# Kernel tuning notes

Measured on AMD Instinct MI355X. Metric: run time of the kernel, lower is better.

The kernel has to match this reference:

```python
import jax, jax.numpy as jnp
import numpy as np

# Dims fixed by ExpertC.__init__ defaults
INPUT_DIM, HIDDEN, OUT_DIM, NLAYERS = 1024, 256, 256, 2
D_STATE, EXPAND, HEADDIM = 32, 2, 32
D_INNER = EXPAND * HIDDEN                      # 512
NHEADS = D_INNER // HEADDIM                    # 16
CONV_DIM = D_INNER + 2 * D_STATE               # 576 (x, B, C; ngroups=1)
D_IN_PROJ = 2 * D_INNER + 2 * D_STATE + NHEADS # 1104 (z, xBC, dt)
KCONV = 4
B, L = 16, 2048
EPS = 1e-5


def setup_inputs() -> dict:
    key = jax.random.key(0)
    ks = iter(jax.random.split(key, 40))
    rn = lambda shape, s: jax.random.normal(next(ks), shape, jnp.float32) * s
    inp = {}
    inp["x"] = rn((B, L, INPUT_DIM), 1.0)
    inp["ip_w"] = rn((INPUT_DIM, HIDDEN), INPUT_DIM ** -0.5)
    inp["ip_b"] = jnp.zeros((HIDDEN,), jnp.float32)
    inp["m_inw"] = rn((NLAYERS, HIDDEN, D_IN_PROJ), HIDDEN ** -0.5)
    inp["m_inb"] = jnp.zeros((NLAYERS, D_IN_PROJ), jnp.float32)
    inp["m_convw"] = rn((NLAYERS, CONV_DIM, KCONV), 0.3)
    inp["m_convb"] = jnp.zeros((NLAYERS, CONV_DIM), jnp.float32)
    inp["m_dtb"] = rn((NLAYERS, NHEADS), 0.5)
    inp["m_Alog"] = jnp.log(1.0 + 15.0 * jax.random.uniform(next(ks), (NLAYERS, NHEADS), jnp.float32))
    inp["m_D"] = jnp.ones((NLAYERS, NHEADS), jnp.float32)
    inp["m_nw"] = jnp.ones((NLAYERS, D_INNER), jnp.float32)
    inp["m_outw"] = rn((NLAYERS, D_INNER, HIDDEN), D_INNER ** -0.5)
    inp["m_outb"] = jnp.zeros((NLAYERS, HIDDEN), jnp.float32)
    inp["rms_w"] = jnp.ones((NLAYERS, HIDDEN), jnp.float32)
    inp["ln1_w"] = jnp.ones((HIDDEN,), jnp.float32)
    inp["ln1_b"] = jnp.zeros((HIDDEN,), jnp.float32)
    inp["w1"] = rn((HIDDEN, 2 * HIDDEN), HIDDEN ** -0.5)
    inp["b1"] = jnp.zeros((2 * HIDDEN,), jnp.float32)
    inp["w2"] = rn((2 * HIDDEN, OUT_DIM), (2 * HIDDEN) ** -0.5)
    inp["b2"] = jnp.zeros((OUT_DIM,), jnp.float32)
    inp["ln2_w"] = jnp.ones((OUT_DIM,), jnp.float32)
    inp["ln2_b"] = jnp.zeros((OUT_DIM,), jnp.float32)
    return inp


def rmsnorm(x, w):
    return x * jax.lax.rsqrt(jnp.mean(x * x, axis=-1, keepdims=True) + EPS) * w


def layernorm(x, w, b):
    m = jnp.mean(x, axis=-1, keepdims=True)
    v = jnp.mean((x - m) ** 2, axis=-1, keepdims=True)
    return (x - m) * jax.lax.rsqrt(v + EPS) * w + b


def mamba_layer(x, inw, inb, convw, convb, dtb, Alog, D, nw, outw, outb):
    b, l, _ = x.shape
    zxbcdt = x @ inw + inb                                   # (b,l,1104)
    z, xBC, dt = jnp.split(zxbcdt, [D_INNER, D_INNER + CONV_DIM], axis=-1)
    dt = jax.nn.softplus(dt + dtb)                           # (b,l,h)
    # causal depthwise conv1d (kernel 4) + silu
    xp = jnp.pad(xBC, ((0, 0), (KCONV - 1, 0), (0, 0)))
    xBC = sum(xp[:, i:i + l, :] * convw[:, i] for i in range(KCONV)) + convb
    xBC = jax.nn.silu(xBC)
    xs, Bm, Cm = jnp.split(xBC, [D_INNER, D_INNER + D_STATE], axis=-1)
    xh = xs.reshape(b, l, NHEADS, HEADDIM)                   # (b,l,h,p)
    A = -jnp.exp(Alog)                                       # (h,)
    dA = jnp.exp(dt * A)                                     # (b,l,h)
    dtx = dt[..., None] * xh                                 # (b,l,h,p)

    def step(h, inp):
        dA_t, dtx_t, B_t, C_t = inp
        # h: (b,h,p,n)
        h = h * dA_t[:, :, None, None] + dtx_t[..., None] * B_t[:, None, None, :]
        y = jnp.einsum('bhpn,bn->bhp', h, C_t)
        return h, y

    h0 = jnp.zeros((b, NHEADS, HEADDIM, D_STATE), x.dtype)
    xs_t = (jnp.moveaxis(dA, 1, 0), jnp.moveaxis(dtx, 1, 0),
            jnp.moveaxis(Bm, 1, 0), jnp.moveaxis(Cm, 1, 0))
    _, ys = jax.lax.scan(step, h0, xs_t)                     # (l,b,h,p)
    y = jnp.moveaxis(ys, 0, 1) + D[None, None, :, None] * xh
    y = y.reshape(b, l, D_INNER)
    y = rmsnorm(y * jax.nn.silu(z), nw)                      # gated RMSNorm
    return y @ outw + outb


def _expert(x, ip_w, ip_b, m_inw, m_inb, m_convw, m_convb, m_dtb, m_Alog, m_D,
            m_nw, m_outw, m_outb, rms_w, ln1_w, ln1_b, w1, b1, w2, b2, ln2_w, ln2_b):
    if x.ndim == 2:
        x = x[:, None, :]
    x = x @ ip_w + ip_b
    for i in range(NLAYERS):
        res = x
        x = mamba_layer(x, m_inw[i], m_inb[i], m_convw[i], m_convb[i], m_dtb[i],
                        m_Alog[i], m_D[i], m_nw[i], m_outw[i], m_outb[i])
        x = rmsnorm(x + res, rms_w[i])
    x = layernorm(x, ln1_w, ln1_b)
    x = jax.nn.gelu(x @ w1 + b1, approximate=False)          # dropout is eval no-op
    x = x @ w2 + b2
    return layernorm(x, ln2_w, ln2_b)


def reference(x, ip_w, ip_b, m_inw, m_inb, m_convw, m_convb, m_dtb, m_Alog, m_D,
              m_nw, m_outw, m_outb, rms_w, ln1_w, ln1_b, w1, b1, w2, b2, ln2_w, ln2_b):
    return _expert(x, ip_w, ip_b, m_inw, m_inb, m_convw, m_convb, m_dtb, m_Alog, m_D,
                   m_nw, m_outw, m_outb, rms_w, ln1_w, ln1_b, w1, b1, w2, b2, ln2_w, ln2_b)
```

## Files before the change

### kernel.cpp

```cpp
#include <hip/hip_runtime.h>

typedef __bf16 bf16;
typedef __bf16 bf16x8 __attribute__((ext_vector_type(8)));
typedef float  f32x4  __attribute__((ext_vector_type(4)));

#define EPSF 1e-5f

__device__ __forceinline__ float bf2f(bf16 x) { return (float)x; }
__device__ __forceinline__ bf16  f2bf(float x) { return (bf16)x; }
__device__ __forceinline__ float siluf(float x) { return x / (1.f + expf(-x)); }

struct PrepackArgs {
    const float* W[7];
    bf16* TH[7];
    bf16* TL[7];
    int K[7];
    int N[7];
};

__global__ __launch_bounds__(256) void prepack_kernel(PrepackArgs a)
{
    int s = blockIdx.y;
    int idx = blockIdx.x * 256 + threadIdx.x;
    int K = a.K[s], N = a.N[s];
    if (idx >= K * N) return;
    int k = idx / N, n = idx - k * N;
    float v = a.W[s][idx];
    bf16 hi = f2bf(v);
    a.TH[s][(size_t)n * K + k] = hi;
    a.TL[s][(size_t)n * K + k] = f2bf(v - bf2f(hi));
}

__global__ __launch_bounds__(256) void gemm_hl(
    const bf16* __restrict__ AH, const bf16* __restrict__ AL,
    const float* __restrict__ Af, int lda,
    const bf16* __restrict__ WTh, const bf16* __restrict__ WTl,
    const float* __restrict__ bias,
    int N, int K,
    float* __restrict__ outF, int ldF,
    bf16* __restrict__ outB, int ldB,
    bf16* __restrict__ outH, bf16* __restrict__ outL, int ldH,
    int doGelu,
    const float* __restrict__ dtb, const float* __restrict__ Alog,
    float* __restrict__ dtf, float* __restrict__ dAf)
{
    __shared__ bf16 As [128][40];
    __shared__ bf16 Als[128][40];

    const int tid  = threadIdx.x;
    const int lane = tid & 63;
    const int wid  = tid >> 6;
    const int waveM = wid & 1, waveN = wid >> 1;
    const int m16 = lane & 15, quad = lane >> 4;
    const int row0 = blockIdx.x * 128;
    const int n0   = blockIdx.y * 64;

    f32x4 acc[4][2];
#pragma unroll
    for (int i = 0; i < 4; ++i)
#pragma unroll
        for (int j = 0; j < 2; ++j)
            acc[i][j] = (f32x4){0.f, 0.f, 0.f, 0.f};

    const int ar = tid >> 1, akc = (tid & 1) * 16;

    const int bn0 = min(n0 + waveN * 32 + m16,      N - 1);
    const int bn1 = min(n0 + waveN * 32 + 16 + m16, N - 1);
    const bf16* bH0p = WTh + (size_t)bn0 * K + quad * 8;
    const bf16* bH1p = WTh + (size_t)bn1 * K + quad * 8;
    const bf16* bL0p = WTl + (size_t)bn0 * K + quad * 8;
    const bf16* bL1p = WTl + (size_t)bn1 * K + quad * 8;

    bf16x8 bH[2], bL[2], bHn[2], bLn[2];
    bH[0] = *(const bf16x8*)(bH0p);
    bH[1] = *(const bf16x8*)(bH1p);
    bL[0] = *(const bf16x8*)(bL0p);
    bL[1] = *(const bf16x8*)(bL1p);

    for (int k0 = 0; k0 < K; k0 += 32) {
        if (AH) {
            const bf16* s0 = AH + (size_t)(row0 + ar) * lda + k0 + akc;
            const bf16* s1 = AL + (size_t)(row0 + ar) * lda + k0 + akc;
            *(uint4*)&As [ar][akc]     = *(const uint4*)s0;
            *(uint4*)&As [ar][akc + 8] = *(const uint4*)(s0 + 8);
            *(uint4*)&Als[ar][akc]     = *(const uint4*)s1;
            *(uint4*)&Als[ar][akc + 8] = *(const uint4*)(s1 + 8);
        } else {
            const float* asrc = Af + (size_t)(row0 + ar) * lda + k0 + akc;
            bf16* dh = &As [ar][akc];
            bf16* dl = &Als[ar][akc];
#pragma unroll
            for (int c = 0; c < 4; ++c) {
                float4 f = ((const float4*)asrc)[c];
#pragma unroll
                for (int e = 0; e < 4; ++e) {
                    float v = (&f.x)[e];
                    bf16 hi = f2bf(v);
                    dh[c * 4 + e] = hi;
                    dl[c * 4 + e] = f2bf(v - bf2f(hi));
                }
            }
        }
        __syncthreads();

        const bool more = (k0 + 32) < K;
        if (more) {
            int kn = k0 + 32;
            bHn[0] = *(const bf16x8*)(bH0p + kn);
            bHn[1] = *(const bf16x8*)(bH1p + kn);
            bLn[0] = *(const bf16x8*)(bL0p + kn);
            bLn[1] = *(const bf16x8*)(bL1p + kn);
        }

        bf16x8 aH[4], aL[4];
#pragma unroll
        for (int mi = 0; mi < 4; ++mi) {
            aH[mi] = *(const bf16x8*)&As [waveM * 64 + mi * 16 + m16][quad * 8];
            aL[mi] = *(const bf16x8*)&Als[waveM * 64 + mi * 16 + m16][quad * 8];
        }

#pragma unroll
        for (int mi = 0; mi < 4; ++mi)
#pragma unroll
            for (int ni = 0; ni < 2; ++ni) {
                acc[mi][ni] = __builtin_amdgcn_mfma_f32_16x16x32_bf16(
                    aH[mi], bH[ni], acc[mi][ni], 0, 0, 0);
                acc[mi][ni] = __builtin_amdgcn_mfma_f32_16x16x32_bf16(
                    aH[mi], bL[ni], acc[mi][ni], 0, 0, 0);
                acc[mi][ni] = __builtin_amdgcn_mfma_f32_16x16x32_bf16(
                    aL[mi], bH[ni], acc[mi][ni], 0, 0, 0);
            }
        __syncthreads();

        if (more) {
            bH[0] = bHn[0]; bH[1] = bHn[1];
            bL[0] = bLn[0]; bL[1] = bLn[1];
        }
    }

#pragma unroll
    for (int ni = 0; ni < 2; ++ni) {
        int col = n0 + waveN * 32 + ni * 16 + m16;
        if (col >= N) continue;
        float bv = bias ? bias[col] : 0.f;
#pragma unroll
        for (int mi = 0; mi < 4; ++mi) {
#pragma unroll
            for (int r = 0; r < 4; ++r) {
                int row = row0 + waveM * 64 + mi * 16 + quad * 4 + r;
                float v = acc[mi][ni][r] + bv;
                if (dtf && col >= 1088) {
                    int head = col - 1088;
                    float xx = v + dtb[head];
                    float sp = (xx > 20.f) ? xx : log1pf(expf(xx));
                    float A  = -expf(Alog[head]);
                    dtf[(size_t)row * 16 + head] = sp;
                    dAf[(size_t)row * 16 + head] = expf(sp * A);
                } else {
                    if (doGelu) v = 0.5f * v * (1.f + erff(v * 0.70710678118654752f));
                    if (outB) outB[(size_t)row * ldB + col] = f2bf(v);
                    if (outF) outF[(size_t)row * ldF + col] = v;
                    if (outH) {
                        bf16 hi = f2bf(v);
                        outH[(size_t)row * ldH + col] = hi;
                        outL[(size_t)row * ldH + col] = f2bf(v - bf2f(hi));
                    }
                }
            }
        }
    }
}

__global__ __launch_bounds__(192) void conv_kernel(
    const bf16* __restrict__ zx,
    const float* __restrict__ cw,
    const float* __restrict__ cb,
    float* __restrict__ xs,
    float* __restrict__ Bc,
    float* __restrict__ Cc)
{
    int row = blockIdx.x;
    int ch  = blockIdx.y * 192 + threadIdx.x;
    int l   = row & 2047;
    float acc = cb[ch];
#pragma unroll
    for (int i = 0; i < 4; ++i) {
        int ls = l + i - 3;
        if (ls >= 0)
            acc += bf2f(zx[(size_t)(row + i - 3) * 1104 + 512 + ch]) * cw[ch * 4 + i];
    }
    float s = siluf(acc);
    if (ch < 512)      xs[(size_t)row * 512 + ch]        = s;
    else if (ch < 544) Bc[(size_t)row * 32 + (ch - 512)] = s;
    else               Cc[(size_t)row * 32 + (ch - 544)] = s;
}

#define QCH   256
#define NCH   8

struct StepB  { float Bv[16]; float da, dtv, xv; };
struct StepBC { float Bv[16]; float Cv[16]; float da, dtv, xv; };

__device__ __forceinline__ void load_stepB(
    StepB& S, const float* Bc, const float* dtf, const float* dAf,
    const float* xs, size_t r, int h, int p, int nb)
{
    const float4* bp = (const float4*)(Bc + r * 32 + nb);
    *(float4*)&S.Bv[0]  = bp[0];
    *(float4*)&S.Bv[4]  = bp[1];
    *(float4*)&S.Bv[8]  = bp[2];
    *(float4*)&S.Bv[12] = bp[3];
    S.da  = dAf[r * 16 + h];
    S.dtv = dtf[r * 16 + h];
    S.xv  = xs[r * 512 + h * 32 + p];
}

__device__ __forceinline__ void load_stepBC(
    StepBC& S, const float* Bc, const float* Cc, const float* dtf,
    const float* dAf, const float* xs, size_t r, int h, int p, int nb)
{
    const float4* bp = (const float4*)(Bc + r * 32 + nb);
    *(float4*)&S.Bv[0]  = bp[0];
    *(float4*)&S.Bv[4]  = bp[1];
    *(float4*)&S.Bv[8]  = bp[2];
    *(float4*)&S.Bv[12] = bp[3];
    const float4* cp = (const float4*)(Cc + r * 32 + nb);
    *(float4*)&S.Cv[0]  = cp[0];
    *(float4*)&S.Cv[4]  = cp[1];
    *(float4*)&S.Cv[8]  = cp[2];
    *(float4*)&S.Cv[12] = cp[3];
    S.da  = dAf[r * 16 + h];
    S.dtv = dtf[r * 16 + h];
    S.xv  = xs[r * 512 + h * 32 + p];
}

__global__ __launch_bounds__(64) void scan_phase1(
    const float* __restrict__ xs,
    const float* __restrict__ Bc,
    const float* __restrict__ dtf,
    const float* __restrict__ dAf,
    float* __restrict__ cs,
    float* __restrict__ cp)
{
    int blk = blockIdx.x;
    int bh = blk >> 3, c = blk & (NCH - 1);
    int b = bh >> 4, h = bh & 15;
    int lane = threadIdx.x;
    int p = lane & 31, half = lane >> 5, nb = half * 16;
    float hs[16];
#pragma unroll
    for (int j = 0; j < 16; ++j) hs[j] = 0.f;
    float P = 1.f;
    size_t rb = (size_t)b * 2048 + (size_t)c * QCH;

    StepB S0, S1;
    load_stepB(S0, Bc, dtf, dAf, xs, rb, h, p, nb);

    for (int t = 0; t < QCH; t += 2) {
        load_stepB(S1, Bc, dtf, dAf, xs, rb + t + 1, h, p, nb);
        {
            float dtx = S0.dtv * S0.xv, da = S0.da;
#pragma unroll
            for (int j = 0; j < 16; ++j)
                hs[j] = fmaf(hs[j], da, dtx * S0.Bv[j]);
            P *= da;
        }
        if (t + 2 < QCH)
            load_stepB(S0, Bc, dtf, dAf, xs, rb + t + 2, h, p, nb);
        {
            float dtx = S1.dtv * S1.xv, da = S1.da;
#pragma unroll
            for (int j = 0; j < 16; ++j)
                hs[j] = fmaf(hs[j], da, dtx * S1.Bv[j]);
            P *= da;
        }
    }

    float* dst = cs + (size_t)blk * 1024 + lane * 16;
#pragma unroll
    for (int q = 0; q < 4; ++q)
        ((float4*)dst)[q] = (float4){hs[q*4], hs[q*4+1], hs[q*4+2], hs[q*4+3]};
    if (lane == 0) cp[blk] = P;
}

__global__ __launch_bounds__(64) void scan_phase2(
    float* __restrict__ cs,
    const float* __restrict__ cp)
{
    int bh = blockIdx.x;
    int lane = threadIdx.x;
    float H[16];
#pragma unroll
    for (int j = 0; j < 16; ++j) H[j] = 0.f;
    for (int c = 0; c < NCH; ++c) {
        float* base = cs + ((size_t)(bh * NCH + c)) * 1024 + lane * 16;
        float E[16];
#pragma unroll
        for (int q = 0; q < 4; ++q) {
            float4 v = ((const float4*)base)[q];
            E[q*4] = v.x; E[q*4+1] = v.y; E[q*4+2] = v.z; E[q*4+3] = v.w;
        }
        float P = cp[bh * NCH + c];
#pragma unroll
        for (int q = 0; q < 4; ++q)
            ((float4*)base)[q] = (float4){H[q*4], H[q*4+1], H[q*4+2], H[q*4+3]};
#pragma unroll
        for (int j = 0; j < 16; ++j)
            H[j] = fmaf(H[j], P, E[j]);
    }
}

__global__ __launch_bounds__(64) void scan_phase3(
    const float* __restrict__ xs,
    const float* __restrict__ Bc,
    const float* __restrict__ Cc,
    const float* __restrict__ dtf,
    const float* __restrict__ dAf,
    const float* __restrict__ Dv,
    const float* __restrict__ cs,
    bf16* __restrict__ y)
{
    int blk = blockIdx.x;
    int bh = blk >> 3, c = blk & (NCH - 1);
    int b = bh >> 4, h = bh & 15;
    int lane = threadIdx.x;
    int p = lane & 31, half = lane >> 5, nb = half * 16;
    float Dh = Dv[h];
    float hs[16];
    {
        const float* src = cs + (size_t)blk * 1024 + lane * 16;
#pragma unroll
        for (int q = 0; q < 4; ++q) {
            float4 v = ((const float4*)src)[q];
            hs[q*4] = v.x; hs[q*4+1] = v.y; hs[q*4+2] = v.z; hs[q*4+3] = v.w;
        }
    }
    size_t rb = (size_t)b * 2048 + (size_t)c * QCH;

    StepBC S0, S1;
    load_stepBC(S0, Bc, Cc, dtf, dAf, xs, rb, h, p, nb);

    for (int t = 0; t < QCH; t += 2) {
        load_stepBC(S1, Bc, Cc, dtf, dAf, xs, rb + t + 1, h, p, nb);
        {
            float dtx = S0.dtv * S0.xv, da = S0.da, yv = 0.f;
#pragma unroll
            for (int j = 0; j < 16; ++j) {
                hs[j] = fmaf(hs[j], da, dtx * S0.Bv[j]);
                yv = fmaf(hs[j], S0.Cv[j], yv);
            }
            yv += __shfl_xor(yv, 32);
            if (half == 0)
                y[(rb + t) * 512 + h * 32 + p] = f2bf(yv + Dh * S0.xv);
        }
        if (t + 2 < QCH)
            load_stepBC(S0, Bc, Cc, dtf, dAf, xs, rb + t + 2, h, p, nb);
        {
            float dtx = S1.dtv * S1.xv, da = S1.da, yv = 0.f;
#pragma unroll
            for (int j = 0; j < 16; ++j) {
                hs[j] = fmaf(hs[j], da, dtx * S1.Bv[j]);
                yv = fmaf(hs[j], S1.Cv[j], yv);
            }
            yv += __shfl_xor(yv, 32);
            if (half == 0)
                y[(rb + t + 1) * 512 + h * 32 + p] = f2bf(yv + Dh * S1.xv);
        }
    }
}

__global__ __launch_bounds__(64) void gaterms_kernel(
    const bf16* __restrict__ y,
    const bf16* __restrict__ zx,
    const float* __restrict__ nw,
    bf16* __restrict__ outH,
    bf16* __restrict__ outL)
{
    int row = blockIdx.x, lane = threadIdx.x;
    union { uint4 u; bf16 b[8]; } yv, zv, oh, ol;
    yv.u = *(const uint4*)(y  + (size_t)row * 512  + lane * 8);
    zv.u = *(const uint4*)(zx + (size_t)row * 1104 + lane * 8);
    float4 nv0 = *(const float4*)(nw + lane * 8);
    float4 nv1 = *(const float4*)(nw + lane * 8 + 4);
    float nvv[8] = {nv0.x, nv0.y, nv0.z, nv0.w, nv1.x, nv1.y, nv1.z, nv1.w};
    float g[8]; float ss = 0.f;
#pragma unroll
    for (int i = 0; i < 8; ++i) {
        float gate = siluf(bf2f(zv.b[i]));
        g[i] = bf2f(yv.b[i]) * gate;
        ss += g[i] * g[i];
    }
#pragma unroll
    for (int o = 1; o < 64; o <<= 1) ss += __shfl_xor(ss, o);
    float rms = rsqrtf(ss * (1.f / 512.f) + EPSF);
#pragma unroll
    for (int i = 0; i < 8; ++i) {
        float v = g[i] * rms * nvv[i];
        bf16 hi = f2bf(v);
        oh.b[i] = hi;
        ol.b[i] = f2bf(v - bf2f(hi));
    }
    *(uint4*)(outH + (size_t)row * 512 + lane * 8) = oh.u;
    *(uint4*)(outL + (size_t)row * 512 + lane * 8) = ol.u;
}

__global__ __launch_bounds__(64) void resrms_kernel(
    const float* __restrict__ mo,
    float* __restrict__ h,
    const float* __restrict__ w)
{
    int row = blockIdx.x, lane = threadIdx.x;
    float4 a = *(const float4*)(mo + (size_t)row * 256 + lane * 4);
    float4 r = *(const float4*)(h  + (size_t)row * 256 + lane * 4);
    float s0 = a.x + r.x, s1 = a.y + r.y, s2 = a.z + r.z, s3 = a.w + r.w;
    float ss = s0 * s0 + s1 * s1 + s2 * s2 + s3 * s3;
#pragma unroll
    for (int o = 1; o < 64; o <<= 1) ss += __shfl_xor(ss, o);
    float rms = rsqrtf(ss * (1.f / 256.f) + EPSF);
    float4 wv = *(const float4*)(w + lane * 4);
    *(float4*)(h + (size_t)row * 256 + lane * 4) =
        (float4){s0 * rms * wv.x, s1 * rms * wv.y, s2 * rms * wv.z, s3 * rms * wv.w};
}

__global__ __launch_bounds__(64) void ln_kernel(
    const float* __restrict__ x,
    const float* __restrict__ w,
    const float* __restrict__ b,
    bf16* __restrict__ outH,
    bf16* __restrict__ outL,
    float* __restrict__ outF)
{
    int row = blockIdx.x, lane = threadIdx.x;
    float4 v = *(const float4*)(x + (size_t)row * 256 + lane * 4);
    float sum = v.x + v.y + v.z + v.w;
    float sq  = v.x * v.x + v.y * v.y + v.z * v.z + v.w * v.w;
#pragma unroll
    for (int o = 1; o < 64; o <<= 1) { sum += __shfl_xor(sum, o); sq += __shfl_xor(sq, o); }
    float m  = sum * (1.f / 256.f);
    float var = sq * (1.f / 256.f) - m * m;
    float is = rsqrtf(var + EPSF);
    float4 wv = *(const float4*)(w + lane * 4);
    float4 bv = *(const float4*)(b + lane * 4);
    float o0 = (v.x - m) * is * wv.x + bv.x;
    float o1 = (v.y - m) * is * wv.y + bv.y;
    float o2 = (v.z - m) * is * wv.z + bv.z;
    float o3 = (v.w - m) * is * wv.w + bv.w;
    if (outH) {
        union { uint2 u; bf16 bb[4]; } oh, ol;
        float o[4] = {o0, o1, o2, o3};
#pragma unroll
        for (int i = 0; i < 4; ++i) {
            bf16 hi = f2bf(o[i]);
            oh.bb[i] = hi;
            ol.bb[i] = f2bf(o[i] - bf2f(hi));
        }
        *(uint2*)(outH + (size_t)row * 256 + lane * 4) = oh.u;
        *(uint2*)(outL + (size_t)row * 256 + lane * 4) = ol.u;
    }
    if (outF)
        *(float4*)(outF + (size_t)row * 256 + lane * 4) = (float4){o0, o1, o2, o3};
}

extern "C" void kernel_launch(void* const* d_in, const int* in_sizes, int n_in,
                              void* d_out, int out_size, void* d_ws, size_t ws_size,
                              hipStream_t stream)
{
    const float* x      = (const float*)d_in[0];
    const float* ip_w   = (const float*)d_in[1];
    const float* ip_b   = (const float*)d_in[2];
    const float* m_inw  = (const float*)d_in[3];
    const float* m_inb  = (const float*)d_in[4];
    const float* m_convw= (const float*)d_in[5];
    const float* m_convb= (const float*)d_in[6];
    const float* m_dtb  = (const float*)d_in[7];
    const float* m_Alog = (const float*)d_in[8];
    const float* m_D    = (const float*)d_in[9];
    const float* m_nw   = (const float*)d_in[10];
    const float* m_outw = (const float*)d_in[11];
    const float* m_outb = (const float*)d_in[12];
    const float* rms_w  = (const float*)d_in[13];
    const float* ln1_w  = (const float*)d_in[14];
    const float* ln1_b  = (const float*)d_in[15];
    const float* w1     = (const float*)d_in[16];
    const float* b1     = (const float*)d_in[17];
    const float* w2     = (const float*)d_in[18];
    const float* b2     = (const float*)d_in[19];
    const float* ln2_w  = (const float*)d_in[20];
    const float* ln2_b  = (const float*)d_in[21];

    const int M = 32768;
    char* wsb = (char*)d_ws;
    size_t off = 0;
    auto alloc = [&](size_t bytes) {
        void* p = wsb + off;
        off += (bytes + 255) & ~(size_t)255;
        return p;
    };
    bf16*  zx   = (bf16*) alloc((size_t)M * 1104 * 2);
    float* h    = (float*)alloc((size_t)M * 256 * 4);
    float* U1   = (float*)alloc((size_t)M * 512 * 4);
    float* Bc   = (float*)alloc((size_t)M * 32 * 4);
    float* Cc   = (float*)alloc((size_t)M * 32 * 4);
    float* dtf  = (float*)alloc((size_t)M * 16 * 4);
    float* dAf  = (float*)alloc((size_t)M * 16 * 4);
    bf16*  ybuf = (bf16*) alloc((size_t)M * 512 * 2);
    float* cs   = (float*)alloc((size_t)2048 * 1024 * 4);
    float* cpb  = (float*)alloc((size_t)2048 * 4);
    bf16* ipTH   = (bf16*)alloc(262144 * 2);
    bf16* ipTL   = (bf16*)alloc(262144 * 2);
    bf16* inwTH0 = (bf16*)alloc(282624 * 2);
    bf16* inwTL0 = (bf16*)alloc(282624 * 2);
    bf16* inwTH1 = (bf16*)alloc(282624 * 2);
    bf16* inwTL1 = (bf16*)alloc(282624 * 2);
    bf16* outwTH0= (bf16*)alloc(131072 * 2);
    bf16* outwTL0= (bf16*)alloc(131072 * 2);
    bf16* outwTH1= (bf16*)alloc(131072 * 2);
    bf16* outwTL1= (bf16*)alloc(131072 * 2);
    bf16* w1TH   = (bf16*)alloc(131072 * 2);
    bf16* w1TL   = (bf16*)alloc(131072 * 2);
    bf16* w2TH   = (bf16*)alloc(131072 * 2);
    bf16* w2TL   = (bf16*)alloc(131072 * 2);
    (void)ws_size; (void)in_sizes; (void)n_in; (void)out_size;

    float* xs      = U1;
    bf16*  normedH = (bf16*)U1;
    bf16*  normedL = normedH + (size_t)M * 512;
    bf16*  tbH     = (bf16*)U1;
    bf16*  tbL     = tbH + (size_t)M * 256;
    float* mo      = (float*)zx;
    bf16*  gH      = (bf16*)zx;
    bf16*  gL      = gH + (size_t)M * 512;
    float* ubuf    = (float*)ybuf;

    PrepackArgs pa;
    pa.W[0] = ip_w;               pa.TH[0] = ipTH;    pa.TL[0] = ipTL;    pa.K[0] = 1024; pa.N[0] = 256;
    pa.W[1] = m_inw;              pa.TH[1] = inwTH0;  pa.TL[1] = inwTL0;  pa.K[1] = 256;  pa.N[1] = 1104;
    pa.W[2] = m_inw + 256*1104;   pa.TH[2] = inwTH1;  pa.TL[2] = inwTL1;  pa.K[2] = 256;  pa.N[2] = 1104;
    pa.W[3] = m_outw;             pa.TH[3] = outwTH0; pa.TL[3] = outwTL0; pa.K[3] = 512;  pa.N[3] = 256;
    pa.W[4] = m_outw + 512*256;   pa.TH[4] = outwTH1; pa.TL[4] = outwTL1; pa.K[4] = 512;  pa.N[4] = 256;
    pa.W[5] = w1;                 pa.TH[5] = w1TH;    pa.TL[5] = w1TL;    pa.K[5] = 256;  pa.N[5] = 512;
    pa.W[6] = w2;                 pa.TH[6] = w2TH;    pa.TL[6] = w2TL;    pa.K[6] = 512;  pa.N[6] = 256;
    prepack_kernel<<<dim3(1104, 7), 256, 0, stream>>>(pa);

    dim3 blk(256);

    gemm_hl<<<dim3(256, 4), blk, 0, stream>>>(
        nullptr, nullptr, x, 1024, ipTH, ipTL, ip_b, 256, 1024,
        h, 256, nullptr, 0, nullptr, nullptr, 0, 0,
        nullptr, nullptr, nullptr, nullptr);

    for (int L = 0; L < 2; ++L) {
        const bf16* inwTH = L ? inwTH1 : inwTH0;
        const bf16* inwTL = L ? inwTL1 : inwTL0;
        const bf16* outwTH= L ? outwTH1 : outwTH0;
        const bf16* outwTL= L ? outwTL1 : outwTL0;
        const float* inb = m_inb  + (size_t)L * 1104;
        const float* cw  = m_convw+ (size_t)L * 576 * 4;
        const float* cb  = m_convb+ (size_t)L * 576;
        const float* dtb = m_dtb  + L * 16;
        const float* Al  = m_Alog + L * 16;
        const float* Dv  = m_D    + L * 16;
        const float* nw  = m_nw   + (size_t)L * 512;
        const float* ob  = m_outb + (size_t)L * 256;
        const float* rw  = rms_w  + (size_t)L * 256;

        gemm_hl<<<dim3(256, 18), blk, 0, stream>>>(
            nullptr, nullptr, h, 256, inwTH, inwTL, inb, 1104, 256,
            nullptr, 0, zx, 1104, nullptr, nullptr, 0, 0,
            dtb, Al, dtf, dAf);
        conv_kernel<<<dim3(M, 3), 192, 0, stream>>>(zx, cw, cb, xs, Bc, Cc);
        scan_phase1<<<2048, 64, 0, stream>>>(xs, Bc, dtf, dAf, cs, cpb);
        scan_phase2<<<256, 64, 0, stream>>>(cs, cpb);
        scan_phase3<<<2048, 64, 0, stream>>>(xs, Bc, Cc, dtf, dAf, Dv, cs, ybuf);
        gaterms_kernel<<<M, 64, 0, stream>>>(ybuf, zx, nw, normedH, normedL);
        gemm_hl<<<dim3(256, 4), blk, 0, stream>>>(
            normedH, normedL, nullptr, 512, outwTH, outwTL, ob, 256, 512,
            mo, 256, nullptr, 0, nullptr, nullptr, 0, 0,
            nullptr, nullptr, nullptr, nullptr);
        resrms_kernel<<<M, 64, 0, stream>>>(mo, h, rw);
    }

    ln_kernel<<<M, 64, 0, stream>>>(h, ln1_w, ln1_b, tbH, tbL, nullptr);
    gemm_hl<<<dim3(256, 8), blk, 0, stream>>>(
        tbH, tbL, nullptr, 256, w1TH, w1TL, b1, 512, 256,
        nullptr, 0, nullptr, 0, gH, gL, 512, 1,
        nullptr, nullptr, nullptr, nullptr);
    gemm_hl<<<dim3(256, 4), blk, 0, stream>>>(
        gH, gL, nullptr, 512, w2TH, w2TL, b2, 256, 512,
        ubuf, 256, nullptr, 0, nullptr, nullptr, 0, 0,
        nullptr, nullptr, nullptr, nullptr);
    ln_kernel<<<M, 64, 0, stream>>>(ubuf, ln2_w, ln2_b, nullptr, nullptr, (float*)d_out);
}
```

Measured before the change: 1.527 ms.

## Split in-proj output buffers, store hidden state as bf16 hi/lo, halve scan chunk

The in-projection epilogue now writes z and xBC into separate contiguous buffers, so the conv and gate kernels read dense rows instead of striding over a 1104-wide row. The residual hidden state is kept as a bf16 hi/lo pair, which lets the in-proj GEMM read the pre-split operand instead of converting fp32 on load; resrms and layernorm are adapted to match. The scan chunk length is halved to 128 with 16 chunks, doubling the block count for phases 1 and 3 to improve occupancy. In exchange, phase 2 does more sequential combine work, and several buffers are now aliased onto one another, which risks overlap hazards.

Result: no change. 1.529 ms (+0.2%).

```diff
diff --git a/kernel.cpp b/kernel.cpp
--- a/kernel.cpp
+++ b/kernel.cpp
@@ -41,6 +41,7 @@
     bf16* __restrict__ outB, int ldB,
     bf16* __restrict__ outH, bf16* __restrict__ outL, int ldH,
     int doGelu,
+    bf16* __restrict__ outZ, bf16* __restrict__ outXBC,
     const float* __restrict__ dtb, const float* __restrict__ Alog,
     float* __restrict__ dtf, float* __restrict__ dAf)
 {
@@ -149,13 +150,19 @@
             for (int r = 0; r < 4; ++r) {
                 int row = row0 + waveM * 64 + mi * 16 + quad * 4 + r;
                 float v = acc[mi][ni][r] + bv;
-                if (dtf && col >= 1088) {
-                    int head = col - 1088;
-                    float xx = v + dtb[head];
-                    float sp = (xx > 20.f) ? xx : log1pf(expf(xx));
-                    float A  = -expf(Alog[head]);
-                    dtf[(size_t)row * 16 + head] = sp;
-                    dAf[(size_t)row * 16 + head] = expf(sp * A);
+                if (outZ) {
+                    if (col < 512) {
+                        outZ[(size_t)row * 512 + col] = f2bf(v);
+                    } else if (col < 1088) {
+                        outXBC[(size_t)row * 576 + (col - 512)] = f2bf(v);
+                    } else {
+                        int head = col - 1088;
+                        float xx = v + dtb[head];
+                        float sp = (xx > 20.f) ? xx : log1pf(expf(xx));
+                        float A  = -expf(Alog[head]);
+                        dtf[(size_t)row * 16 + head] = sp;
+                        dAf[(size_t)row * 16 + head] = expf(sp * A);
+                    }
                 } else {
                     if (doGelu) v = 0.5f * v * (1.f + erff(v * 0.70710678118654752f));
                     if (outB) outB[(size_t)row * ldB + col] = f2bf(v);
@@ -172,7 +179,7 @@
 }
 
 __global__ __launch_bounds__(192) void conv_kernel(
-    const bf16* __restrict__ zx,
+    const bf16* __restrict__ xbc,
     const float* __restrict__ cw,
     const float* __restrict__ cb,
     float* __restrict__ xs,
@@ -187,7 +194,7 @@
     for (int i = 0; i < 4; ++i) {
         int ls = l + i - 3;
         if (ls >= 0)
-            acc += bf2f(zx[(size_t)(row + i - 3) * 1104 + 512 + ch]) * cw[ch * 4 + i];
+            acc += bf2f(xbc[(size_t)(row + i - 3) * 576 + ch]) * cw[ch * 4 + i];
     }
     float s = siluf(acc);
     if (ch < 512)      xs[(size_t)row * 512 + ch]        = s;
@@ -195,8 +202,8 @@
     else               Cc[(size_t)row * 32 + (ch - 544)] = s;
 }
 
-#define QCH   256
-#define NCH   8
+#define QCH   128
+#define NCH   16
 
 struct StepB  { float Bv[16]; float da, dtv, xv; };
 struct StepBC { float Bv[16]; float Cv[16]; float da, dtv, xv; };
@@ -243,7 +250,7 @@
     float* __restrict__ cp)
 {
     int blk = blockIdx.x;
-    int bh = blk >> 3, c = blk & (NCH - 1);
+    int bh = blk >> 4, c = blk & (NCH - 1);
     int b = bh >> 4, h = bh & 15;
     int lane = threadIdx.x;
     int p = lane & 31, half = lane >> 5, nb = half * 16;
@@ -321,7 +328,7 @@
     bf16* __restrict__ y)
 {
     int blk = blockIdx.x;
-    int bh = blk >> 3, c = blk & (NCH - 1);
+    int bh = blk >> 4, c = blk & (NCH - 1);
     int b = bh >> 4, h = bh & 15;
     int lane = threadIdx.x;
     int p = lane & 31, half = lane >> 5, nb = half * 16;
@@ -371,15 +378,15 @@
 
 __global__ __launch_bounds__(64) void gaterms_kernel(
     const bf16* __restrict__ y,
-    const bf16* __restrict__ zx,
+    const bf16* __restrict__ z,
     const float* __restrict__ nw,
     bf16* __restrict__ outH,
     bf16* __restrict__ outL)
 {
     int row = blockIdx.x, lane = threadIdx.x;
     union { uint4 u; bf16 b[8]; } yv, zv, oh, ol;
-    yv.u = *(const uint4*)(y  + (size_t)row * 512  + lane * 8);
-    zv.u = *(const uint4*)(zx + (size_t)row * 1104 + lane * 8);
+    yv.u = *(const uint4*)(y + (size_t)row * 512 + lane * 8);
+    zv.u = *(const uint4*)(z + (size_t)row * 512 + lane * 8);
     float4 nv0 = *(const float4*)(nw + lane * 8);
     float4 nv1 = *(const float4*)(nw + lane * 8 + 4);
     float nvv[8] = {nv0.x, nv0.y, nv0.z, nv0.w, nv1.x, nv1.y, nv1.z, nv1.w};
@@ -406,24 +413,40 @@
 
 __global__ __launch_bounds__(64) void resrms_kernel(
     const float* __restrict__ mo,
-    float* __restrict__ h,
+    bf16* __restrict__ hH,
+    bf16* __restrict__ hL,
     const float* __restrict__ w)
 {
     int row = blockIdx.x, lane = threadIdx.x;
     float4 a = *(const float4*)(mo + (size_t)row * 256 + lane * 4);
-    float4 r = *(const float4*)(h  + (size_t)row * 256 + lane * 4);
-    float s0 = a.x + r.x, s1 = a.y + r.y, s2 = a.z + r.z, s3 = a.w + r.w;
-    float ss = s0 * s0 + s1 * s1 + s2 * s2 + s3 * s3;
+    union { uint2 u; bf16 b[4]; } hv, lv;
+    hv.u = *(const uint2*)(hH + (size_t)row * 256 + lane * 4);
+    lv.u = *(const uint2*)(hL + (size_t)row * 256 + lane * 4);
+    float s[4];
+    s[0] = a.x + bf2f(hv.b[0]) + bf2f(lv.b[0]);
+    s[1] = a.y + bf2f(hv.b[1]) + bf2f(lv.b[1]);
+    s[2] = a.z + bf2f(hv.b[2]) + bf2f(lv.b[2]);
+    s[3] = a.w + bf2f(hv.b[3]) + bf2f(lv.b[3]);
+    float ss = s[0]*s[0] + s[1]*s[1] + s[2]*s[2] + s[3]*s[3];
 #pragma unroll
     for (int o = 1; o < 64; o <<= 1) ss += __shfl_xor(ss, o);
     float rms = rsqrtf(ss * (1.f / 256.f) + EPSF);
     float4 wv = *(const float4*)(w + lane * 4);
-    *(float4*)(h + (size_t)row * 256 + lane * 4) =
-        (float4){s0 * rms * wv.x, s1 * rms * wv.y, s2 * rms * wv.z, s3 * rms * wv.w};
+    float o[4] = {s[0]*rms*wv.x, s[1]*rms*wv.y, s[2]*rms*wv.z, s[3]*rms*wv.w};
+    union { uint2 u; bf16 b[4]; } oh, ol;
+#pragma unroll
+    for (int i = 0; i < 4; ++i) {
+        bf16 hi = f2bf(o[i]);
+        oh.b[i] = hi;
+        ol.b[i] = f2bf(o[i] - bf2f(hi));
+    }
+    *(uint2*)(hH + (size_t)row * 256 + lane * 4) = oh.u;
+    *(uint2*)(hL + (size_t)row * 256 + lane * 4) = ol.u;
 }
 
 __global__ __launch_bounds__(64) void ln_kernel(
-    const float* __restrict__ x,
+    const float* __restrict__ xF,
+    const bf16* __restrict__ xHi, const bf16* __restrict__ xLo,
     const float* __restrict__ w,
     const float* __restrict__ b,
     bf16* __restrict__ outH,
@@ -431,9 +454,21 @@
     float* __restrict__ outF)
 {
     int row = blockIdx.x, lane = threadIdx.x;
-    float4 v = *(const float4*)(x + (size_t)row * 256 + lane * 4);
-    float sum = v.x + v.y + v.z + v.w;
-    float sq  = v.x * v.x + v.y * v.y + v.z * v.z + v.w * v.w;
+    float v0, v1, v2, v3;
+    if (xF) {
+        float4 v = *(const float4*)(xF + (size_t)row * 256 + lane * 4);
+        v0 = v.x; v1 = v.y; v2 = v.z; v3 = v.w;
+    } else {
+        union { uint2 u; bf16 b[4]; } hv, lv;
+        hv.u = *(const uint2*)(xHi + (size_t)row * 256 + lane * 4);
+        lv.u = *(const uint2*)(xLo + (size_t)row * 256 + lane * 4);
+        v0 = bf2f(hv.b[0]) + bf2f(lv.b[0]);
+        v1 = bf2f(hv.b[1]) + bf2f(lv.b[1]);
+        v2 = bf2f(hv.b[2]) + bf2f(lv.b[2]);
+        v3 = bf2f(hv.b[3]) + bf2f(lv.b[3]);
+    }
+    float sum = v0 + v1 + v2 + v3;
+    float sq  = v0*v0 + v1*v1 + v2*v2 + v3*v3;
 #pragma unroll
     for (int o = 1; o < 64; o <<= 1) { sum += __shfl_xor(sum, o); sq += __shfl_xor(sq, o); }
     float m  = sum * (1.f / 256.f);
@@ -441,10 +476,10 @@
     float is = rsqrtf(var + EPSF);
     float4 wv = *(const float4*)(w + lane * 4);
     float4 bv = *(const float4*)(b + lane * 4);
-    float o0 = (v.x - m) * is * wv.x + bv.x;
-    float o1 = (v.y - m) * is * wv.y + bv.y;
-    float o2 = (v.z - m) * is * wv.z + bv.z;
-    float o3 = (v.w - m) * is * wv.w + bv.w;
+    float o0 = (v0 - m) * is * wv.x + bv.x;
+    float o1 = (v1 - m) * is * wv.y + bv.y;
+    float o2 = (v2 - m) * is * wv.z + bv.z;
+    float o3 = (v3 - m) * is * wv.w + bv.w;
     if (outH) {
         union { uint2 u; bf16 bb[4]; } oh, ol;
         float o[4] = {o0, o1, o2, o3};
@@ -496,16 +531,17 @@
         off += (bytes + 255) & ~(size_t)255;
         return p;
     };
-    bf16*  zx   = (bf16*) alloc((size_t)M * 1104 * 2);
-    float* h    = (float*)alloc((size_t)M * 256 * 4);
+    bf16*  zb   = (bf16*) alloc((size_t)M * 512 * 2);
+    bf16*  xbc  = (bf16*) alloc((size_t)M * 576 * 2);
+    bf16*  hH   = (bf16*) alloc((size_t)M * 256 * 2);
+    bf16*  hL   = (bf16*) alloc((size_t)M * 256 * 2);
     float* U1   = (float*)alloc((size_t)M * 512 * 4);
     float* Bc   = (float*)alloc((size_t)M * 32 * 4);
     float* Cc   = (float*)alloc((size_t)M * 32 * 4);
     float* dtf  = (float*)alloc((size_t)M * 16 * 4);
     float* dAf  = (float*)alloc((size_t)M * 16 * 4);
     bf16*  ybuf = (bf16*) alloc((size_t)M * 512 * 2);
-    float* cs   = (float*)alloc((size_t)2048 * 1024 * 4);
-    float* cpb  = (float*)alloc((size_t)2048 * 4);
+    float* cpb  = (float*)alloc((size_t)4096 * 4);
     bf16* ipTH   = (bf16*)alloc(262144 * 2);
     bf16* ipTL   = (bf16*)alloc(262144 * 2);
     bf16* inwTH0 = (bf16*)alloc(282624 * 2);
@@ -527,9 +563,10 @@
     bf16*  normedL = normedH + (size_t)M * 512;
     bf16*  tbH     = (bf16*)U1;
     bf16*  tbL     = tbH + (size_t)M * 256;
-    float* mo      = (float*)zx;
-    bf16*  gH      = (bf16*)zx;
-    bf16*  gL      = gH + (size_t)M * 512;
+    float* cs      = (float*)xbc;
+    float* mo      = (float*)xbc;
+    bf16*  gH      = zb;
+    bf16*  gL      = xbc;
     float* ubuf    = (float*)ybuf;
 
     PrepackArgs pa;
@@ -546,8 +583,8 @@
 
     gemm_hl<<<dim3(256, 4), blk, 0, stream>>>(
         nullptr, nullptr, x, 1024, ipTH, ipTL, ip_b, 256, 1024,
-        h, 256, nullptr, 0, nullptr, nullptr, 0, 0,
-        nullptr, nullptr, nullptr, nullptr);
+        nullptr, 0, nullptr, 0, hH, hL, 256, 0,
+        nullptr, nullptr, nullptr, nullptr, nullptr, nullptr);
 
     for (int L = 0; L < 2; ++L) {
         const bf16* inwTH = L ? inwTH1 : inwTH0;
@@ -565,29 +602,30 @@
         const float* rw  = rms_w  + (size_t)L * 256;
 
         gemm_hl<<<dim3(256, 18), blk, 0, stream>>>(
-            nullptr, nullptr, h, 256, inwTH, inwTL, inb, 1104, 256,
-            nullptr, 0, zx, 1104, nullptr, nullptr, 0, 0,
-            dtb, Al, dtf, dAf);
-        conv_kernel<<<dim3(M, 3), 192, 0, stream>>>(zx, cw, cb, xs, Bc, Cc);
-        scan_phase1<<<2048, 64, 0, stream>>>(xs, Bc, dtf, dAf, cs, cpb);
+            hH, hL, nullptr, 256, inwTH, inwTL, inb, 1104, 256,
+            nullptr, 0, nullptr, 0, nullptr, nullptr, 0, 0,
+            zb, xbc, dtb, Al, dtf, dAf);
+        conv_kernel<<<dim3(M, 3), 192, 0, stream>>>(xbc, cw, cb, xs, Bc, Cc);
+        scan_phase1<<<4096, 64, 0, stream>>>(xs, Bc, dtf, dAf, cs, cpb);
         scan_phase2<<<256, 64, 0, stream>>>(cs, cpb);
-        scan_phase3<<<2048, 64, 0, stream>>>(xs, Bc, Cc, dtf, dAf, Dv, cs, ybuf);
-        gaterms_kernel<<<M, 64, 0, stream>>>(ybuf, zx, nw, normedH, normedL);
+        scan_phase3<<<4096, 64, 0, stream>>>(xs, Bc, Cc, dtf, dAf, Dv, cs, ybuf);
+        gaterms_kernel<<<M, 64, 0, stream>>>(ybuf, zb, nw, normedH, normedL);
         gemm_hl<<<dim3(256, 4), blk, 0, stream>>>(
             normedH, normedL, nullptr, 512, outwTH, outwTL, ob, 256, 512,
             mo, 256, nullptr, 0, nullptr, nullptr, 0, 0,
-            nullptr, nullptr, nullptr, nullptr);
-        resrms_kernel<<<M, 64, 0, stream>>>(mo, h, rw);
-    }
-
-    ln_kernel<<<M, 64, 0, stream>>>(h, ln1_w, ln1_b, tbH, tbL, nullptr);
+            nullptr, nullptr, nullptr, nullptr, nullptr, nullptr);
+        resrms_kernel<<<M, 64, 0, stream>>>(mo, hH, hL, rw);
+    }
+
+    ln_kernel<<<M, 64, 0, stream>>>(nullptr, hH, hL, ln1_w, ln1_b, tbH, tbL, nullptr);
     gemm_hl<<<dim3(256, 8), blk, 0, stream>>>(
         tbH, tbL, nullptr, 256, w1TH, w1TL, b1, 512, 256,
         nullptr, 0, nullptr, 0, gH, gL, 512, 1,
-        nullptr, nullptr, nullptr, nullptr);
+        nullptr, nullptr, nullptr, nullptr, nullptr, nullptr);
     gemm_hl<<<dim3(256, 4), blk, 0, stream>>>(
         gH, gL, nullptr, 512, w2TH, w2TL, b2, 256, 512,
         ubuf, 256, nullptr, 0, nullptr, nullptr, 0, 0,
-        nullptr, nullptr, nullptr, nullptr);
-    ln_kernel<<<M, 64, 0, stream>>>(ubuf, ln2_w, ln2_b, nullptr, nullptr, (float*)d_out);
-}
+        nullptr, nullptr, nullptr, nullptr, nullptr, nullptr);
+    ln_kernel<<<M, 64, 0, stream>>>(ubuf, nullptr, nullptr, ln2_w, ln2_b,
+                                    nullptr, nullptr, (float*)d_out);
+}
```
